# Kernel tuning notes

Hardware: AMD Instinct MI355X
Metric: run time of the kernel (lower is better)

## Reference

```python
import jax, jax.numpy as jnp
import numpy as np
import math


def haar_dwt(x):
    # x: [B, C, H, W] -> (LL [B,C,H/2,W/2], bands [B,C,3,H/2,W/2]) orthogonal Haar
    B, C, H, W = x.shape
    xr = x.reshape(B, C, H // 2, 2, W // 2, 2)
    a = xr[:, :, :, 0, :, 0]
    b = xr[:, :, :, 0, :, 1]
    c = xr[:, :, :, 1, :, 0]
    d = xr[:, :, :, 1, :, 1]
    ll = (a + b + c + d) * 0.5
    lh = (a + b - c - d) * 0.5  # horizontal detail
    hl = (a - b + c - d) * 0.5  # vertical detail
    hh = (a - b - c + d) * 0.5  # diagonal detail
    return ll, jnp.stack([lh, hl, hh], axis=2)


def haar_idwt(ll, bands):
    # inverse of haar_dwt (perfect reconstruction)
    lh, hl, hh = bands[:, :, 0], bands[:, :, 1], bands[:, :, 2]
    a = (ll + lh + hl + hh) * 0.5
    b = (ll + lh - hl - hh) * 0.5
    c = (ll - lh + hl - hh) * 0.5
    d = (ll - lh - hl + hh) * 0.5
    B, C, h, w = ll.shape
    out = jnp.stack([jnp.stack([a, b], -1), jnp.stack([c, d], -1)], -3)  # [B,C,h,2,w,2]
    return out.reshape(B, C, 2 * h, 2 * w)


def selective_scan(u, prompt, x_proj_w, dt_proj_w, dt_proj_b, A_logs, Ds):
    # u: [B, L, C] input sequence; prompt: [B, L, N] added to C projection
    B, L, C = u.shape
    R = dt_proj_w.shape[1]
    N = A_logs.shape[1]
    x_dbl = jnp.einsum('blc,rc->blr', u, x_proj_w)            # [B, L, R+2N]
    dts, Bs, Cs = jnp.split(x_dbl, [R, R + N], axis=-1)        # [B,L,R], [B,L,N], [B,L,N]
    delta = jax.nn.softplus(jnp.einsum('blr,cr->blc', dts, dt_proj_w) + dt_proj_b)  # [B,L,C]
    Cs = Cs + prompt
    A = -jnp.exp(A_logs)                                       # [C, N]
    # time-major for scan
    delta_t = jnp.moveaxis(delta, 1, 0)                        # [L,B,C]
    u_t = jnp.moveaxis(u, 1, 0)                                # [L,B,C]
    Bs_t = jnp.moveaxis(Bs, 1, 0)                              # [L,B,N]
    Cs_t = jnp.moveaxis(Cs, 1, 0)                              # [L,B,N]
    dA = jnp.exp(delta_t[..., None] * A)                       # [L,B,C,N]
    dBu = delta_t[..., None] * Bs_t[:, :, None, :] * u_t[..., None]  # [L,B,C,N]

    def step(h, inp):
        dA_l, dBu_l, C_l = inp
        h = dA_l * h + dBu_l
        y = jnp.einsum('bcn,bn->bc', h, C_l)
        return h, y

    h0 = jnp.zeros((B, C, N), dtype=u.dtype)
    _, ys = jax.lax.scan(step, h0, (dA, dBu, Cs_t))            # ys: [L,B,C]
    y = jnp.moveaxis(ys, 0, 1)                                 # [B,L,C]
    return y + u * Ds


def setup_inputs() -> dict:
    B, H, W, C, N = 4, 128, 128, 128, 8
    R = math.ceil(C / 16)  # dt_rank = 8
    L = H * W
    key = jax.random.key(0)
    ks = jax.random.split(key, 10)
    x = jax.random.normal(ks[0], (B, L, C), jnp.float32)
    prompt = jax.random.normal(ks[1], (B, L, N), jnp.float32) * 0.1
    in_proj_w = jax.random.normal(ks[2], (2 * C, C), jnp.float32) * (C ** -0.5)
    x_proj_w = jax.random.normal(ks[3], (R + 2 * N, C), jnp.float32) * (C ** -0.5)
    std = R ** -0.5
    dt_proj_w = jax.random.uniform(ks[4], (C, R), jnp.float32, minval=-std, maxval=std)
    dt = jnp.clip(jnp.exp(jax.random.uniform(ks[5], (C,), jnp.float32)
                          * (math.log(0.1) - math.log(0.001)) + math.log(0.001)), 1e-4)
    dt_proj_b = dt + jnp.log(-jnp.expm1(-dt))  # inverse softplus init
    A_logs = jnp.broadcast_to(jnp.log(jnp.arange(1, N + 1, dtype=jnp.float32)), (C, N)).copy()
    Ds = jnp.ones((C,), jnp.float32)
    ln_gamma = jnp.ones((C,), jnp.float32)
    ln_beta = jnp.zeros((C,), jnp.float32)
    out_proj_w = jax.random.normal(ks[6], (C, C), jnp.float32) * (C ** -0.5)
    out_proj_b = jnp.zeros((C,), jnp.float32)
    return dict(x=x, prompt=prompt, in_proj_w=in_proj_w, x_proj_w=x_proj_w,
                dt_proj_w=dt_proj_w, dt_proj_b=dt_proj_b, A_logs=A_logs, Ds=Ds,
                ln_gamma=ln_gamma, ln_beta=ln_beta, out_proj_w=out_proj_w,
                out_proj_b=out_proj_b, H=H, W=W)


def reference(x, prompt, in_proj_w, x_proj_w, dt_proj_w, dt_proj_b, A_logs, Ds,
              ln_gamma, ln_beta, out_proj_w, out_proj_b, H, W):
    B, L, C = x.shape
    xz = x @ in_proj_w.T                                       # [B,L,2C]
    x_proc, z = jnp.split(xz, 2, axis=-1)
    prepare = x_proc.reshape(B, H, W, C).transpose(0, 3, 1, 2)  # [B,C,H,W]
    # J=2 Haar DWT
    Yl1, bands1 = haar_dwt(prepare)                            # level 1: H/2
    Yl2, bands2 = haar_dwt(Yl1)                                # level 2: H/4
    h2, w2 = H // 4, W // 4
    # pack coarsest level into top-left quadrants of a zero canvas (as original)
    h00 = jnp.zeros_like(prepare)
    h00 = h00.at[:, :, :h2, :w2].set(Yl2)
    h00 = h00.at[:, :, :h2, w2:2 * w2].set(bands2[:, :, 0])
    h00 = h00.at[:, :, h2:2 * h2, :w2].set(bands2[:, :, 1])
    h00 = h00.at[:, :, h2:2 * h2, w2:2 * w2].set(bands2[:, :, 2])
    h00_seq = h00.transpose(0, 2, 3, 1).reshape(B, L, C)
    # Mamba-style selective scan over the wavelet-domain sequence
    h11_seq = selective_scan(h00_seq, prompt, x_proj_w, dt_proj_w, dt_proj_b, A_logs, Ds)
    h11 = h11_seq.reshape(B, H, W, C).transpose(0, 3, 1, 2)
    # unpack scanned coarsest level; level-1 details kept as-is
    Yl2n = h11[:, :, :h2, :w2]
    bands2n = jnp.stack([h11[:, :, :h2, w2:2 * w2],
                         h11[:, :, h2:2 * h2, :w2],
                         h11[:, :, h2:2 * h2, w2:2 * w2]], axis=2)
    Yl1n = haar_idwt(Yl2n, bands2n)
    recons = haar_idwt(Yl1n, bands1)                           # [B,C,H,W]
    y = recons.transpose(0, 2, 3, 1).reshape(B, L, C)
    # LayerNorm over channels
    mu = jnp.mean(y, axis=-1, keepdims=True)
    var = jnp.var(y, axis=-1, keepdims=True)
    y = (y - mu) * jax.lax.rsqrt(var + 1e-5) * ln_gamma + ln_beta
    # SiLU gate + output projection + residual
    y = y * jax.nn.silu(z)
    out = y @ out_proj_w.T + out_proj_b
    return out + x
```

## Files before the change

### kernel.cpp

```cpp
#include <hip/hip_runtime.h>

#define B_   4
#define H_   128
#define W_   128
#define L_   (H_*W_)
#define C_   128
#define N_   8
#define R_   8
#define LS_  4096
#define CS_  16
#define NC_  256

#define OFF_XPROC 0ull
#define OFF_Z     (OFF_XPROC + (size_t)B_*L_*C_)
#define OFF_BANDS (OFF_Z     + (size_t)B_*L_*C_)
#define OFF_U     (OFF_BANDS + (size_t)B_*3*64*64*C_)
#define OFF_DELTA (OFF_U     + (size_t)B_*LS_*C_)
#define OFF_BS    (OFF_DELTA + (size_t)B_*LS_*C_)
#define OFF_CS    (OFF_BS    + (size_t)B_*LS_*N_)
#define OFF_DSUM  (OFF_CS    + (size_t)B_*LS_*N_)
#define OFF_HEND  (OFF_DSUM  + (size_t)B_*NC_*C_)
#define OFF_HIN   (OFF_HEND  + (size_t)B_*NC_*C_*N_)
#define OFF_H11   (OFF_HIN   + (size_t)B_*NC_*C_*N_)
#define OFF_WCVT  (OFF_H11   + (size_t)B_*LS_*C_)

typedef __attribute__((ext_vector_type(8))) short bf16x8;
typedef __attribute__((ext_vector_type(4))) float f32x4;

__device__ __forceinline__ float softplus_f(float x) {
    return (x > 20.f) ? x : log1pf(__expf(x));
}

__device__ __forceinline__ void split_bf16(float x, short& h, short& l) {
    const unsigned u  = __float_as_uint(x);
    const unsigned hr = (u + 0x7FFFu + ((u >> 16) & 1u)) >> 16;
    h = (short)hr;
    const float hf = __uint_as_float(hr << 16);
    l = (short)(__float_as_uint(x - hf) >> 16);
}

__device__ __forceinline__ f32x4 mfma16(bf16x8 a, bf16x8 b, f32x4 c) {
    return __builtin_amdgcn_mfma_f32_16x16x32_bf16(a, b, c, 0, 0, 0);
}

__global__ __launch_bounds__(256) void k_cvt(const float* __restrict__ w_in,
        const float* __restrict__ w_out, unsigned short* __restrict__ wq) {
    const int i = blockIdx.x * 256 + threadIdx.x;
    float v; unsigned short *hi, *lo; int idx;
    if (i < 32768) { v = w_in[i];          hi = wq;         lo = wq + 32768; idx = i; }
    else           { v = w_out[i - 32768]; hi = wq + 65536; lo = wq + 81920; idx = i - 32768; }
    short h, l; split_bf16(v, h, l);
    hi[idx] = (unsigned short)h;
    lo[idx] = (unsigned short)l;
}

template<bool EPI>
__global__ __launch_bounds__(256) void k_gemm_mfma(const float* __restrict__ in,
        const unsigned short* __restrict__ whi, const unsigned short* __restrict__ wlo,
        float* __restrict__ out0, float* __restrict__ out1,
        const float* __restrict__ bias, const float* __restrict__ resid) {
    const int tid  = threadIdx.x;
    const int wave = tid >> 6, lane = tid & 63;
    const int lrow = lane & 15;
    const int lk8  = (lane >> 4) << 3;
    int r0, c0;
    if constexpr (EPI) { r0 = blockIdx.x * 64 + (wave >> 1) * 32; c0 = (wave & 1) * 64; }
    else               { r0 = blockIdx.x * 32;                    c0 = wave * 64; }

    f32x4 acc[2][4];
    #pragma unroll
    for (int rb = 0; rb < 2; ++rb)
        #pragma unroll
        for (int cb = 0; cb < 4; ++cb)
            acc[rb][cb] = (f32x4){0.f, 0.f, 0.f, 0.f};

    const float* a0 = in + (size_t)(r0 + lrow) * C_ + lk8;
    const float* a1 = in + (size_t)(r0 + 16 + lrow) * C_ + lk8;

    #pragma unroll
    for (int ks = 0; ks < 4; ++ks) {
        bf16x8 ah[2], al[2];
        #pragma unroll
        for (int rb = 0; rb < 2; ++rb) {
            const float* ap = (rb ? a1 : a0) + ks * 32;
            const float4 v0 = *(const float4*)ap;
            const float4 v1 = *(const float4*)(ap + 4);
            const float f[8] = {v0.x, v0.y, v0.z, v0.w, v1.x, v1.y, v1.z, v1.w};
            #pragma unroll
            for (int i = 0; i < 8; ++i) {
                short h, l; split_bf16(f[i], h, l);
                ah[rb][i] = h; al[rb][i] = l;
            }
        }
        #pragma unroll
        for (int cb = 0; cb < 4; ++cb) {
            const size_t boff = (size_t)(c0 + cb * 16 + lrow) * C_ + ks * 32 + lk8;
            const bf16x8 bh = *(const bf16x8*)(whi + boff);
            const bf16x8 bl = *(const bf16x8*)(wlo + boff);
            #pragma unroll
            for (int rb = 0; rb < 2; ++rb) {
                f32x4 t = acc[rb][cb];
                t = mfma16(ah[rb], bh, t);
                t = mfma16(ah[rb], bl, t);
                t = mfma16(al[rb], bh, t);
                acc[rb][cb] = t;
            }
        }
    }
    #pragma unroll
    for (int rb = 0; rb < 2; ++rb)
        #pragma unroll
        for (int cb = 0; cb < 4; ++cb) {
            const int col = c0 + cb * 16 + lrow;
            float* op; int colo;
            if constexpr (EPI) { op = out0; colo = col; }
            else { const bool toz = (c0 + cb * 16) >= 128; op = toz ? out1 : out0; colo = col & 127; }
            const float bz = EPI ? bias[colo] : 0.f;
            #pragma unroll
            for (int j = 0; j < 4; ++j) {
                const size_t row = (size_t)r0 + rb * 16 + (lane >> 4) * 4 + j;
                float v = acc[rb][cb][j] + bz;
                if constexpr (EPI) v += resid[row * C_ + colo];
                op[row * C_ + colo] = v;
            }
        }
}

__global__ __launch_bounds__(128) void k_dwt(const float* __restrict__ xp,
        float* __restrict__ bands, float* __restrict__ u) {
    const int c = threadIdx.x;
    const int bid = blockIdx.x;
    const int b = bid >> 10, p = (bid >> 5) & 31, q = bid & 31;
    float v[4][4];
    const size_t base = (size_t)b * L_ * C_ + c;
    #pragma unroll
    for (int i = 0; i < 4; ++i)
        #pragma unroll
        for (int j = 0; j < 4; ++j)
            v[i][j] = xp[base + (size_t)(((p<<2)+i)*W_ + (q<<2)+j) * C_];
    const size_t bstride = (size_t)64*64*C_;
    float ll[2][2];
    #pragma unroll
    for (int di = 0; di < 2; ++di)
        #pragma unroll
        for (int dj = 0; dj < 2; ++dj) {
            const float a  = v[2*di][2*dj],   bb = v[2*di][2*dj+1];
            const float cc = v[2*di+1][2*dj], dd = v[2*di+1][2*dj+1];
            ll[di][dj]     = (a+bb+cc+dd)*0.5f;
            const float lh = (a+bb-cc-dd)*0.5f;
            const float hl = (a-bb+cc-dd)*0.5f;
            const float hh = (a-bb-cc+dd)*0.5f;
            const int i1 = (p<<1)+di, j1 = (q<<1)+dj;
            const size_t bb0 = (((size_t)b*3*64 + i1)*64 + j1)*C_ + c;
            bands[bb0]             = lh;
            bands[bb0 +   bstride] = hl;
            bands[bb0 + 2*bstride] = hh;
        }
    const float a = ll[0][0], bb = ll[0][1], cc = ll[1][0], dd = ll[1][1];
    const float l2  = (a+bb+cc+dd)*0.5f;
    const float lh2 = (a+bb-cc-dd)*0.5f;
    const float hl2 = (a-bb+cc-dd)*0.5f;
    const float hh2 = (a-bb-cc+dd)*0.5f;
    const size_t ub = (size_t)b*LS_*C_ + c;
    u[ub + (size_t)((p<<6)+q)*C_]          = l2;
    u[ub + (size_t)((p<<6)+32+q)*C_]       = lh2;
    u[ub + (size_t)(((32+p)<<6)+q)*C_]     = hl2;
    u[ub + (size_t)(((32+p)<<6)+32+q)*C_]  = hh2;
}

__global__ __launch_bounds__(256) void k_prep(const float* __restrict__ u,
        const float* __restrict__ prompt, const float* __restrict__ xw,
        const float* __restrict__ dtw, const float* __restrict__ dtb,
        float* __restrict__ delta, float* __restrict__ Bsv, float* __restrict__ Csv) {
    __shared__ float us[64*133];
    __shared__ float xws[128*26];
    __shared__ float xdbl[64*26];
    const int tid = threadIdx.x;
    const int b = blockIdx.x >> 6;
    const int s0 = (blockIdx.x & 63) << 6;
    {
        const int pp = tid >> 5, k4 = (tid & 31) << 2;
        #pragma unroll
        for (int i = 0; i < 8; ++i) {
            const int pos = pp + (i << 3);
            const float4 v = *(const float4*)(u + ((size_t)b*LS_ + s0 + pos)*C_ + k4);
            us[pos*133 + k4 + 0] = v.x;
            us[pos*133 + k4 + 1] = v.y;
            us[pos*133 + k4 + 2] = v.z;
            us[pos*133 + k4 + 3] = v.w;
        }
    }
    for (int idx = tid; idx < 128*24; idx += 256) {
        const int k = idx / 24, r = idx - k*24;
        xws[k*26 + r] = xw[r*C_ + k];
    }
    __syncthreads();
    {
        const int pos = tid & 63, ty = tid >> 6;
        float acc[6] = {0.f,0.f,0.f,0.f,0.f,0.f};
        for (int k = 0; k < 128; ++k) {
            const float a = us[pos*133 + k];
            #pragma unroll
            for (int rr = 0; rr < 6; ++rr)
                acc[rr] += a * xws[k*26 + ty*6 + rr];
        }
        #pragma unroll
        for (int rr = 0; rr < 6; ++rr) xdbl[pos*26 + ty*6 + rr] = acc[rr];
    }
    __syncthreads();
    {
        const int c = tid & 127, ph = tid >> 7;
        float wreg[8];
        *(float4*)&wreg[0] = *(const float4*)(dtw + c*8);
        *(float4*)&wreg[4] = *(const float4*)(dtw + c*8 + 4);
        const float bb = dtb[c];
        for (int i = 0; i < 32; ++i) {
            const int pos = ph*32 + i;
            float dd = bb;
            #pragma unroll
            for (int r = 0; r < 8; ++r) dd += xdbl[pos*26 + r] * wreg[r];
            delta[((size_t)b*LS_ + s0 + pos)*C_ + c] = softplus_f(dd);
        }
    }
    #pragma unroll
    for (int i = 0; i < 2; ++i) {
        const int idx = (i << 8) + tid;
        const int pos = idx >> 3, n = idx & 7;
        const int s = s0 + pos;
        const int l = ((s >> 6) << 7) | (s & 63);
        Bsv[((size_t)b*LS_ + s)*N_ + n] = xdbl[pos*26 + 8 + n];
        Csv[((size_t)b*LS_ + s)*N_ + n] = xdbl[pos*26 + 16 + n]
                                        + prompt[((size_t)b*L_ + l)*N_ + n];
    }
}

__global__ __launch_bounds__(256) void k_scan1(const float* __restrict__ delta,
        const float* __restrict__ u, const float* __restrict__ Bsv,
        const float* __restrict__ Alog, float* __restrict__ dsum, float* __restrict__ hend) {
    const int tid = threadIdx.x;
    const int b = blockIdx.x >> 7, k2 = blockIdx.x & 127;
    const int k = (k2 << 1) | (tid >> 7);
    const int c = tid & 127;
    float al[8];
    *(float4*)&al[0] = *(const float4*)(Alog + c*8);
    *(float4*)&al[4] = *(const float4*)(Alog + c*8 + 4);
    float an[8];
    #pragma unroll
    for (int n = 0; n < 8; ++n) an[n] = -__expf(al[n]);
    float h[8] = {0,0,0,0,0,0,0,0};
    float cum = 0.f;
    const int s0 = k << 4;
    for (int t = 0; t < CS_; ++t) {
        const int s = s0 + t;
        const size_t base = ((size_t)b*LS_ + s)*C_ + c;
        const float d  = delta[base];
        const float uu = u[base];
        float bv[8];
        const float4* bp = (const float4*)(Bsv + ((size_t)b*LS_ + s)*N_);
        *(float4*)&bv[0] = bp[0];
        *(float4*)&bv[4] = bp[1];
        cum += d;
        const float du = d * uu;
        #pragma unroll
        for (int n = 0; n < 8; ++n)
            h[n] = __expf(d*an[n])*h[n] + bv[n]*du;
    }
    const size_t idx = (size_t)(b*NC_ + k)*C_ + c;
    dsum[idx] = cum;
    *(float4*)(hend + idx*N_)     = make_float4(h[0],h[1],h[2],h[3]);
    *(float4*)(hend + idx*N_ + 4) = make_float4(h[4],h[5],h[6],h[7]);
}

#define KB_ 16
__global__ __launch_bounds__(256) void k_comb(const float* __restrict__ dsum,
        const float* __restrict__ hend, const float* __restrict__ Alog,
        const float* __restrict__ dtb, float* __restrict__ hin) {
    const int g = blockIdx.x * 256 + threadIdx.x;
    const int b = g >> 10;
    const int c = (g >> 3) & 127;
    const int n = g & 7;
    const float a  = -__expf(Alog[c*N_ + n]);
    const float d0 = softplus_f(dtb[c]);
    const float dz = __expf(a * (64.f * d0));
    float carry = 0.f;
    float ea[KB_], ha[KB_], eb[KB_], hb[KB_];
    auto LOAD = [&](int kb, float* e, float* hv) {
        #pragma unroll
        for (int j = 0; j < KB_; ++j) {
            const size_t idx = (size_t)(b*NC_ + kb + j)*C_ + c;
            e[j]  = a * dsum[idx];
            hv[j] = hend[idx*N_ + n];
        }
    };
    auto CHAIN = [&](int kb, const float* e, const float* hv) {
        #pragma unroll
        for (int j = 0; j < KB_; ++j) {
            const int k = kb + j;
            if (k && !(k & 3)) carry *= dz;
            hin[((size_t)(b*NC_ + k)*C_ + c)*N_ + n] = carry;
            carry = __expf(e[j])*carry + hv[j];
        }
    };
    LOAD(0, ea, ha);
    for (int kb = 0; kb < NC_; kb += 2*KB_) {
        LOAD(kb + KB_, eb, hb);
        CHAIN(kb, ea, ha);
        if (kb + 2*KB_ < NC_) LOAD(kb + 2*KB_, ea, ha);
        CHAIN(kb + KB_, eb, hb);
    }
}

__global__ __launch_bounds__(256) void k_scan2(const float* __restrict__ delta,
        const float* __restrict__ u, const float* __restrict__ Bsv,
        const float* __restrict__ Csv, const float* __restrict__ Alog,
        const float* __restrict__ Ds, const float* __restrict__ hin,
        float* __restrict__ h11) {
    const int tid = threadIdx.x;
    const int b = blockIdx.x >> 7, k2 = blockIdx.x & 127;
    const int k = (k2 << 1) | (tid >> 7);
    const int c = tid & 127;
    float al[8];
    *(float4*)&al[0] = *(const float4*)(Alog + c*8);
    *(float4*)&al[4] = *(const float4*)(Alog + c*8 + 4);
    float an[8];
    #pragma unroll
    for (int n = 0; n < 8; ++n) an[n] = -__expf(al[n]);
    float h[8];
    const float4* hp = (const float4*)(hin + ((size_t)(b*NC_ + k)*C_ + c)*N_);
    *(float4*)&h[0] = hp[0];
    *(float4*)&h[4] = hp[1];
    const float dsc = Ds[c];
    const int s0 = k << 4;
    for (int t = 0; t < CS_; ++t) {
        const int s = s0 + t;
        const size_t base = ((size_t)b*LS_ + s)*C_ + c;
        const float d  = delta[base];
        const float uu = u[base];
        float bv[8], cv[8];
        const float4* bp = (const float4*)(Bsv + ((size_t)b*LS_ + s)*N_);
        const float4* cp = (const float4*)(Csv + ((size_t)b*LS_ + s)*N_);
        *(float4*)&bv[0] = bp[0];
        *(float4*)&bv[4] = bp[1];
        *(float4*)&cv[0] = cp[0];
        *(float4*)&cv[4] = cp[1];
        const float du = d * uu;
        float y = uu * dsc;
        #pragma unroll
        for (int n = 0; n < 8; ++n) {
            h[n] = __expf(d*an[n])*h[n] + bv[n]*du;
            y += h[n] * cv[n];
        }
        h11[base] = y;
    }
}

__global__ __launch_bounds__(128) void k_idwt_ln(const float* __restrict__ h11,
        const float* __restrict__ bands, const float* __restrict__ z,
        const float* __restrict__ gamma, const float* __restrict__ beta,
        float* __restrict__ yout) {
    __shared__ float vb[16][129];
    __shared__ float stat[16][2];
    const int c = threadIdx.x;
    const int bid = blockIdx.x;
    const int b = bid >> 10, p = (bid >> 5) & 31, q = bid & 31;
    const size_t ub = (size_t)b*LS_*C_ + c;
    const float l2  = h11[ub + (size_t)((p<<6)+q)*C_];
    const float lh2 = h11[ub + (size_t)((p<<6)+32+q)*C_];
    const float hl2 = h11[ub + (size_t)(((32+p)<<6)+q)*C_];
    const float hh2 = h11[ub + (size_t)(((32+p)<<6)+32+q)*C_];
    float yl1[2][2];
    yl1[0][0] = (l2+lh2+hl2+hh2)*0.5f;
    yl1[0][1] = (l2+lh2-hl2-hh2)*0.5f;
    yl1[1][0] = (l2-lh2+hl2-hh2)*0.5f;
    yl1[1][1] = (l2-lh2-hl2+hh2)*0.5f;
    const size_t bstride = (size_t)64*64*C_;
    float v[16];
    #pragma unroll
    for (int di = 0; di < 2; ++di)
        #pragma unroll
        for (int dj = 0; dj < 2; ++dj) {
            const int i1 = (p<<1)+di, j1 = (q<<1)+dj;
            const size_t bb0 = (((size_t)b*3*64 + i1)*64 + j1)*C_ + c;
            const float lh = bands[bb0];
            const float hl = bands[bb0 +   bstride];
            const float hh = bands[bb0 + 2*bstride];
            const float ll = yl1[di][dj];
            v[(2*di+0)*4 + 2*dj+0] = (ll+lh+hl+hh)*0.5f;
            v[(2*di+0)*4 + 2*dj+1] = (ll+lh-hl-hh)*0.5f;
            v[(2*di+1)*4 + 2*dj+0] = (ll-lh+hl-hh)*0.5f;
            v[(2*di+1)*4 + 2*dj+1] = (ll-lh-hl+hh)*0.5f;
        }
    #pragma unroll
    for (int p16 = 0; p16 < 16; ++p16) vb[p16][c] = v[p16];
    __syncthreads();
    {
        const int pp = c >> 3, gg = c & 7;
        float s = 0.f, ss = 0.f;
        #pragma unroll
        for (int i = 0; i < 16; ++i) {
            const float x = vb[pp][gg*16 + i];
            s += x; ss += x*x;
        }
        s += __shfl_xor(s, 1); ss += __shfl_xor(ss, 1);
        s += __shfl_xor(s, 2); ss += __shfl_xor(ss, 2);
        s += __shfl_xor(s, 4); ss += __shfl_xor(ss, 4);
        if (gg == 0) { stat[pp][0] = s; stat[pp][1] = ss; }
    }
    __syncthreads();
    const float gm = gamma[c], bt = beta[c];
    #pragma unroll
    for (int p16 = 0; p16 < 16; ++p16) {
        const int lr = p16 >> 2, lc = p16 & 3;
        const size_t l = (size_t)((p<<2)+lr)*W_ + (q<<2)+lc;
        const float mu  = stat[p16][0] * 0.0078125f;
        const float var = stat[p16][1] * 0.0078125f - mu*mu;
        const float ri  = rsqrtf(var + 1e-5f);
        float y = (v[p16] - mu)*ri*gm + bt;
        const float zv = z[((size_t)b*L_ + l)*C_ + c];
        y *= zv / (1.f + __expf(-zv));
        yout[((size_t)b*L_ + l)*C_ + c] = y;
    }
}

extern "C" void kernel_launch(void* const* d_in, const int* in_sizes, int n_in,
                              void* d_out, int out_size, void* d_ws, size_t ws_size,
                              hipStream_t stream) {
    (void)in_sizes; (void)n_in; (void)out_size; (void)ws_size;
    const float* x      = (const float*)d_in[0];
    const float* prompt = (const float*)d_in[1];
    const float* in_w   = (const float*)d_in[2];
    const float* x_w    = (const float*)d_in[3];
    const float* dt_w   = (const float*)d_in[4];
    const float* dt_b   = (const float*)d_in[5];
    const float* A_logs = (const float*)d_in[6];
    const float* Ds     = (const float*)d_in[7];
    const float* gam    = (const float*)d_in[8];
    const float* bet    = (const float*)d_in[9];
    const float* out_w  = (const float*)d_in[10];
    const float* out_b  = (const float*)d_in[11];
    float* wsp   = (float*)d_ws;
    float* xproc = wsp + OFF_XPROC;
    float* z     = wsp + OFF_Z;
    float* bands = wsp + OFF_BANDS;
    float* u     = wsp + OFF_U;
    float* delta = wsp + OFF_DELTA;
    float* Bs    = wsp + OFF_BS;
    float* Cs    = wsp + OFF_CS;
    float* dsum  = wsp + OFF_DSUM;
    float* hend  = wsp + OFF_HEND;
    float* hin   = wsp + OFF_HIN;
    float* h11   = wsp + OFF_H11;
    unsigned short* wq = (unsigned short*)(wsp + OFF_WCVT);
    unsigned short* whi_in  = wq;
    unsigned short* wlo_in  = wq + 32768;
    unsigned short* whi_out = wq + 65536;
    unsigned short* wlo_out = wq + 81920;
    float* out   = (float*)d_out;

    k_cvt<<<192, 256, 0, stream>>>(in_w, out_w, wq);
    k_gemm_mfma<false><<<2048, 256, 0, stream>>>(x, whi_in, wlo_in, xproc, z, nullptr, nullptr);
    k_dwt<<<4096, 128, 0, stream>>>(xproc, bands, u);
    k_prep<<<256, 256, 0, stream>>>(u, x_w ? prompt : prompt, x_w, dt_w, dt_b, delta, Bs, Cs);
    k_scan1<<<512, 256, 0, stream>>>(delta, u, Bs, A_logs, dsum, hend);
    k_comb<<<16, 256, 0, stream>>>(dsum, hend, A_logs, dt_b, hin);
    k_scan2<<<512, 256, 0, stream>>>(delta, u, Bs, Cs, A_logs, Ds, hin, h11);
    k_idwt_ln<<<4096, 128, 0, stream>>>(h11, bands, z, gam, bet, xproc);
    k_gemm_mfma<true><<<1024, 256, 0, stream>>>(xproc, whi_out, wlo_out, out, nullptr, out_b, x);
}
```

Before: 260.9 us.

## Split x_proj prep into split-bf16 MFMA GEMM plus elementwise delta/B/C kernel

Replaces the shared-memory scalar-FMA k_prep kernel with two kernels. k_xdbl computes the x_proj projection (128→24, padded to 32 columns) using split-bf16 MFMA instructions (three products per tile to keep near-fp32 accuracy), with the weights pre-split in k_cvt. k_dbc then computes delta (softplus), Bs and Cs+prompt elementwise from the stored x_dbl rows. The intent is to move the dominant projection onto matrix cores and raise parallelism. The cost is an extra kernel launch and a global round trip for the 32-wide x_dbl buffer.

```diff
diff --git a/kernel.cpp b/kernel.cpp
--- a/kernel.cpp
+++ b/kernel.cpp
@@ -10,6 +10,7 @@
 #define LS_  4096
 #define CS_  16
 #define NC_  256
+#define ST_  (B_*LS_)
 
 #define OFF_XPROC 0ull
 #define OFF_Z     (OFF_XPROC + (size_t)B_*L_*C_)
@@ -22,7 +23,8 @@
 #define OFF_HEND  (OFF_DSUM  + (size_t)B_*NC_*C_)
 #define OFF_HIN   (OFF_HEND  + (size_t)B_*NC_*C_*N_)
 #define OFF_H11   (OFF_HIN   + (size_t)B_*NC_*C_*N_)
-#define OFF_WCVT  (OFF_H11   + (size_t)B_*LS_*C_)
+#define OFF_XDBL  (OFF_H11   + (size_t)B_*LS_*C_)
+#define OFF_WCVT  (OFF_XDBL  + (size_t)ST_*32)
 
 typedef __attribute__((ext_vector_type(8))) short bf16x8;
 typedef __attribute__((ext_vector_type(4))) float f32x4;
@@ -44,11 +46,17 @@
 }
 
 __global__ __launch_bounds__(256) void k_cvt(const float* __restrict__ w_in,
-        const float* __restrict__ w_out, unsigned short* __restrict__ wq) {
+        const float* __restrict__ w_out, const float* __restrict__ xw,
+        unsigned short* __restrict__ wq) {
     const int i = blockIdx.x * 256 + threadIdx.x;
     float v; unsigned short *hi, *lo; int idx;
-    if (i < 32768) { v = w_in[i];          hi = wq;         lo = wq + 32768; idx = i; }
-    else           { v = w_out[i - 32768]; hi = wq + 65536; lo = wq + 81920; idx = i - 32768; }
+    if (i < 32768)      { v = w_in[i];          hi = wq;         lo = wq + 32768;  idx = i; }
+    else if (i < 49152) { v = w_out[i - 32768]; hi = wq + 65536; lo = wq + 81920;  idx = i - 32768; }
+    else {
+        idx = i - 49152;
+        v = (idx < 24*128) ? xw[idx] : 0.f;
+        hi = wq + 98304; lo = wq + 102400;
+    }
     short h, l; split_bf16(v, h, l);
     hi[idx] = (unsigned short)h;
     lo[idx] = (unsigned short)l;
@@ -126,6 +134,93 @@
         }
 }
 
+__global__ __launch_bounds__(256) void k_xdbl(const float* __restrict__ u,
+        const unsigned short* __restrict__ xwhi, const unsigned short* __restrict__ xwlo,
+        float* __restrict__ xd) {
+    const int tid  = threadIdx.x;
+    const int wave = tid >> 6, lane = tid & 63;
+    const int lrow = lane & 15;
+    const int lk8  = (lane >> 4) << 3;
+    const int r0   = blockIdx.x * 128 + wave * 32;
+
+    f32x4 acc[2][2];
+    #pragma unroll
+    for (int rb = 0; rb < 2; ++rb)
+        #pragma unroll
+        for (int cb = 0; cb < 2; ++cb)
+            acc[rb][cb] = (f32x4){0.f, 0.f, 0.f, 0.f};
+
+    const float* a0 = u + (size_t)(r0 + lrow) * C_ + lk8;
+    const float* a1 = u + (size_t)(r0 + 16 + lrow) * C_ + lk8;
+
+    #pragma unroll
+    for (int ks = 0; ks < 4; ++ks) {
+        bf16x8 ah[2], al[2];
+        #pragma unroll
+        for (int rb = 0; rb < 2; ++rb) {
+            const float* ap = (rb ? a1 : a0) + ks * 32;
+            const float4 v0 = *(const float4*)ap;
+            const float4 v1 = *(const float4*)(ap + 4);
+            const float f[8] = {v0.x, v0.y, v0.z, v0.w, v1.x, v1.y, v1.z, v1.w};
+            #pragma unroll
+            for (int i = 0; i < 8; ++i) {
+                short h, l; split_bf16(f[i], h, l);
+                ah[rb][i] = h; al[rb][i] = l;
+            }
+        }
+        #pragma unroll
+        for (int cb = 0; cb < 2; ++cb) {
+            const size_t boff = (size_t)(cb * 16 + lrow) * C_ + ks * 32 + lk8;
+            const bf16x8 bh = *(const bf16x8*)(xwhi + boff);
+            const bf16x8 bl = *(const bf16x8*)(xwlo + boff);
+            #pragma unroll
+            for (int rb = 0; rb < 2; ++rb) {
+                f32x4 t = acc[rb][cb];
+                t = mfma16(ah[rb], bh, t);
+                t = mfma16(ah[rb], bl, t);
+                t = mfma16(al[rb], bh, t);
+                acc[rb][cb] = t;
+            }
+        }
+    }
+    #pragma unroll
+    for (int rb = 0; rb < 2; ++rb)
+        #pragma unroll
+        for (int cb = 0; cb < 2; ++cb) {
+            const int col = cb * 16 + lrow;
+            #pragma unroll
+            for (int j = 0; j < 4; ++j) {
+                const int row = r0 + rb * 16 + (lane >> 4) * 4 + j;
+                xd[(size_t)row * 32 + col] = acc[rb][cb][j];
+            }
+        }
+}
+
+__global__ __launch_bounds__(256) void k_dbc(const float* __restrict__ xd,
+        const float* __restrict__ prompt, const float* __restrict__ dtw,
+        const float* __restrict__ dtb, float* __restrict__ delta,
+        float* __restrict__ Bsv, float* __restrict__ Csv) {
+    const int tid = threadIdx.x;
+    const int g = blockIdx.x * 2 + (tid >> 7);
+    const int c = tid & 127;
+    const float* xr = xd + (size_t)g * 32;
+    float wreg[8];
+    *(float4*)&wreg[0] = *(const float4*)(dtw + c*8);
+    *(float4*)&wreg[4] = *(const float4*)(dtw + c*8 + 4);
+    float dd = dtb[c];
+    #pragma unroll
+    for (int r = 0; r < 8; ++r) dd += xr[r] * wreg[r];
+    delta[(size_t)g * C_ + c] = softplus_f(dd);
+    if (c < 8) {
+        Bsv[(size_t)g * N_ + c] = xr[8 + c];
+    } else if (c < 16) {
+        const int n = c - 8;
+        const int b = g >> 12, s = g & 4095;
+        const int l = ((s >> 6) << 7) | (s & 63);
+        Csv[(size_t)g * N_ + n] = xr[16 + n] + prompt[((size_t)b*L_ + l)*N_ + n];
+    }
+}
+
 __global__ __launch_bounds__(128) void k_dwt(const float* __restrict__ xp,
         float* __restrict__ bands, float* __restrict__ u) {
     const int c = threadIdx.x;
@@ -166,72 +261,6 @@
     u[ub + (size_t)((p<<6)+32+q)*C_]       = lh2;
     u[ub + (size_t)(((32+p)<<6)+q)*C_]     = hl2;
     u[ub + (size_t)(((32+p)<<6)+32+q)*C_]  = hh2;
-}
-
-__global__ __launch_bounds__(256) void k_prep(const float* __restrict__ u,
-        const float* __restrict__ prompt, const float* __restrict__ xw,
-        const float* __restrict__ dtw, const float* __restrict__ dtb,
-        float* __restrict__ delta, float* __restrict__ Bsv, float* __restrict__ Csv) {
-    __shared__ float us[64*133];
-    __shared__ float xws[128*26];
-    __shared__ float xdbl[64*26];
-    const int tid = threadIdx.x;
-    const int b = blockIdx.x >> 6;
-    const int s0 = (blockIdx.x & 63) << 6;
-    {
-        const int pp = tid >> 5, k4 = (tid & 31) << 2;
-        #pragma unroll
-        for (int i = 0; i < 8; ++i) {
-            const int pos = pp + (i << 3);
-            const float4 v = *(const float4*)(u + ((size_t)b*LS_ + s0 + pos)*C_ + k4);
-            us[pos*133 + k4 + 0] = v.x;
-            us[pos*133 + k4 + 1] = v.y;
-            us[pos*133 + k4 + 2] = v.z;
-            us[pos*133 + k4 + 3] = v.w;
-        }
-    }
-    for (int idx = tid; idx < 128*24; idx += 256) {
-        const int k = idx / 24, r = idx - k*24;
-        xws[k*26 + r] = xw[r*C_ + k];
-    }
-    __syncthreads();
-    {
-        const int pos = tid & 63, ty = tid >> 6;
-        float acc[6] = {0.f,0.f,0.f,0.f,0.f,0.f};
-        for (int k = 0; k < 128; ++k) {
-            const float a = us[pos*133 + k];
-            #pragma unroll
-            for (int rr = 0; rr < 6; ++rr)
-                acc[rr] += a * xws[k*26 + ty*6 + rr];
-        }
-        #pragma unroll
-        for (int rr = 0; rr < 6; ++rr) xdbl[pos*26 + ty*6 + rr] = acc[rr];
-    }
-    __syncthreads();
-    {
-        const int c = tid & 127, ph = tid >> 7;
-        float wreg[8];
-        *(float4*)&wreg[0] = *(const float4*)(dtw + c*8);
-        *(float4*)&wreg[4] = *(const float4*)(dtw + c*8 + 4);
-        const float bb = dtb[c];
-        for (int i = 0; i < 32; ++i) {
-            const int pos = ph*32 + i;
-            float dd = bb;
-            #pragma unroll
-            for (int r = 0; r < 8; ++r) dd += xdbl[pos*26 + r] * wreg[r];
-            delta[((size_t)b*LS_ + s0 + pos)*C_ + c] = softplus_f(dd);
-        }
-    }
-    #pragma unroll
-    for (int i = 0; i < 2; ++i) {
-        const int idx = (i << 8) + tid;
-        const int pos = idx >> 3, n = idx & 7;
-        const int s = s0 + pos;
-        const int l = ((s >> 6) << 7) | (s & 63);
-        Bsv[((size_t)b*LS_ + s)*N_ + n] = xdbl[pos*26 + 8 + n];
-        Csv[((size_t)b*LS_ + s)*N_ + n] = xdbl[pos*26 + 16 + n]
-                                        + prompt[((size_t)b*L_ + l)*N_ + n];
-    }
 }
 
 __global__ __launch_bounds__(256) void k_scan1(const float* __restrict__ delta,
@@ -450,17 +479,21 @@
     float* hend  = wsp + OFF_HEND;
     float* hin   = wsp + OFF_HIN;
     float* h11   = wsp + OFF_H11;
+    float* xd    = wsp + OFF_XDBL;
     unsigned short* wq = (unsigned short*)(wsp + OFF_WCVT);
     unsigned short* whi_in  = wq;
     unsigned short* wlo_in  = wq + 32768;
     unsigned short* whi_out = wq + 65536;
     unsigned short* wlo_out = wq + 81920;
+    unsigned short* whi_xw  = wq + 98304;
+    unsigned short* wlo_xw  = wq + 102400;
     float* out   = (float*)d_out;
 
-    k_cvt<<<192, 256, 0, stream>>>(in_w, out_w, wq);
+    k_cvt<<<208, 256, 0, stream>>>(in_w, out_w, x_w, wq);
     k_gemm_mfma<false><<<2048, 256, 0, stream>>>(x, whi_in, wlo_in, xproc, z, nullptr, nullptr);
     k_dwt<<<4096, 128, 0, stream>>>(xproc, bands, u);
-    k_prep<<<256, 256, 0, stream>>>(u, x_w ? prompt : prompt, x_w, dt_w, dt_b, delta, Bs, Cs);
+    k_xdbl<<<128, 256, 0, stream>>>(u, whi_xw, wlo_xw, xd);
+    k_dbc<<<8192, 256, 0, stream>>>(xd, prompt, dt_w, dt_b, delta, Bs, Cs);
     k_scan1<<<512, 256, 0, stream>>>(delta, u, Bs, A_logs, dsum, hend);
     k_comb<<<16, 256, 0, stream>>>(dsum, hend, A_logs, dt_b, hin);
     k_scan2<<<512, 256, 0, stream>>>(delta, u, Bs, Cs, A_logs, Ds, hin, h11);
```

After: 258.0 us. About the same (-1.1%).
